# Kernel optimization log

Hardware: AMD Instinct MI355X
Metric: run time of the kernel (lower is better)

Reference implementation:

```python
import jax, jax.numpy as jnp
import numpy as np

B, C, H, W = 4, 64, 256, 256
P = 4           # patch_size
PRIOR = 64      # prior_dim
HID = 128       # token_embed_dim (score-net hidden)
E = 128         # attention embed dim
NH = 4          # num_heads
RATIO = 0.25    # top-k keep ratio (amp == phase)
TOK = C * P * P                 # 1024 token dim
SFEAT = 2 * TOK + 2 + PRIOR     # score-net input dim


def setup_inputs():
    ks = jax.random.split(jax.random.key(0), 24)
    g = lambda i, s, sc=0.02: jax.random.normal(ks[i], s, jnp.float32) * sc
    z = lambda n: jnp.zeros((n,), jnp.float32)
    return dict(
        vis_feat=g(0, (B, C, H, W), 1.0), ir_feat=g(1, (B, C, H, W), 1.0),
        prompt_bank=g(2, (4, PRIOR), 0.1),
        Wr=g(3, (2 * C, PRIOR)), br=z(PRIOR),
        aW1=g(4, (SFEAT, HID)), ab1=z(HID), aW2=g(5, (HID, 1)), ab2=z(1),
        aWq=g(6, (TOK, E)), aWk=g(7, (TOK, E)), aWv=g(8, (TOK, E)), aWo=g(9, (E, TOK)),
        pW1=g(10, (SFEAT, HID)), pb1=z(HID), pW2=g(11, (HID, 1)), pb2=z(1),
        pWq=g(12, (TOK, E)), pWk=g(13, (TOK, E)), pWv=g(14, (TOK, E)), pWo=g(15, (E, TOK)),
        c1w=g(16, (C, C, 3, 3)), c1b=z(C), c2w=g(17, (C, C, 3, 3)), c2b=z(C))


def _patchify(x):
    b, c, h, w = x.shape
    hp, wp = h // P, w // P
    t = x.reshape(b, c, hp, P, wp, P).transpose(0, 2, 4, 1, 3, 5).reshape(b, hp * wp, c * P * P)
    return t, hp, wp


def _unpatchify(t, hp, wp):
    b = t.shape[0]
    return t.reshape(b, hp, wp, C, P, P).transpose(0, 3, 1, 4, 2, 5).reshape(b, C, hp * P, wp * P)


def _coords(hp, wp):
    ys, xs = jnp.meshgrid(jnp.arange(hp, dtype=jnp.float32), jnp.arange(wp, dtype=jnp.float32), indexing='ij')
    return jnp.stack([ys / (hp - 1), xs / (wp - 1)], -1).reshape(hp * wp, 2)


def _mha(q_tok, kv_tok, Wq, Wk, Wv, Wo):
    # cross-attention: queries from vis-selected, keys/values from ir-selected
    b, k, _ = q_tok.shape
    dh = E // NH
    q = (q_tok @ Wq).reshape(b, k, NH, dh).transpose(0, 2, 1, 3)
    kk = (kv_tok @ Wk).reshape(b, k, NH, dh).transpose(0, 2, 1, 3)
    v = (kv_tok @ Wv).reshape(b, k, NH, dh).transpose(0, 2, 1, 3)
    att = jax.nn.softmax(jnp.einsum('bhqd,bhkd->bhqk', q, kk) * (1.0 / np.sqrt(dh)), -1)
    o = jnp.einsum('bhqk,bhkd->bhqd', att, v).transpose(0, 2, 1, 3).reshape(b, k, E)
    return q_tok + o @ Wo  # residual back to token dim


def _fuse_branch(vis_map, ir_map, intent, W1, b1, W2, b2, Wq, Wk, Wv, Wo):
    vt, hp, wp = _patchify(vis_map)   # [B,N,TOK]
    it, _, _ = _patchify(ir_map)
    b, n, _ = vt.shape
    cds = jnp.broadcast_to(_coords(hp, wp), (b, n, 2))
    ib = jnp.broadcast_to(intent[:, None, :], (b, n, PRIOR))
    feat = jnp.concatenate([vt, it, cds, ib], -1)        # [B,N,SFEAT]
    score = (jax.nn.relu(feat @ W1 + b1) @ W2 + b2)[..., 0]  # [B,N]
    k = int(n * RATIO)
    _, idx = jax.lax.top_k(score, k)                     # [B,k]
    vs = jnp.take_along_axis(vt, idx[..., None], 1)      # gather selected tokens
    irs = jnp.take_along_axis(it, idx[..., None], 1)
    fs = _mha(vs, irs, Wq, Wk, Wv, Wo)                   # fuse selected via attention
    full = 0.5 * (vt + it)                               # average for unselected
    full = full.at[jnp.arange(b)[:, None], idx].set(fs)  # scatter fused back
    return _unpatchify(full, hp, wp)


def _conv3(x, w, b):
    return jax.lax.conv_general_dilated(x, w, (1, 1), 'SAME', dimension_numbers=('NCHW', 'OIHW', 'NCHW')) + b[None, :, None, None]


def reference(vis_feat, ir_feat, prompt_bank, Wr, br,
              aW1, ab1, aW2, ab2, aWq, aWk, aWv, aWo,
              pW1, pb1, pW2, pb2, pWq, pWk, pWv, pWo,
              c1w, c1b, c2w, c2b):
    # intent router: GAP both modalities -> project -> softmax over prompt bank
    gv = vis_feat.mean((2, 3))
    gi = ir_feat.mean((2, 3))
    pf = jnp.concatenate([gv, gi], -1) @ Wr + br         # [B,PRIOR]
    wts = jax.nn.softmax(pf @ prompt_bank.T, -1)
    intent = wts @ prompt_bank                           # [B,PRIOR]
    # split amplitude/phase via 2D FFT
    Fv = jnp.fft.fft2(vis_feat)
    Fi = jnp.fft.fft2(ir_feat)
    va, vp = jnp.abs(Fv), jnp.angle(Fv)
    ia, ip = jnp.abs(Fi), jnp.angle(Fi)
    fa = _fuse_branch(va, ia, intent, aW1, ab1, aW2, ab2, aWq, aWk, aWv, aWo)
    fp = _fuse_branch(vp, ip, intent, pW1, pb1, pW2, pb2, pWq, pWk, pWv, pWo)
    fp = jnp.arctan2(jnp.sin(fp), jnp.cos(fp))           # phase wrap to (-pi, pi]
    spatial = jnp.fft.ifft2(fa * jnp.exp(1j * fp)).real.astype(jnp.float32)
    r = jax.nn.relu(_conv3(spatial, c1w, c1b))
    r = _conv3(r, c2w, c2b)
    return r + 0.5 * (vis_feat + ir_feat)
```

## Files before the change

kernel.cpp:

```cpp
#include <hip/hip_runtime.h>
#include <hip/hip_bf16.h>
#include <math.h>


#define PI2F 6.28318530717958647692f
#define WS_NEED 178348032ull

__device__ __forceinline__ float bf(const __hip_bfloat16 x) { return __bfloat162float(x); }
__device__ __forceinline__ float ldin(const void* p, size_t i, int f32) {
  return f32 ? ((const float*)p)[i] : bf(((const __hip_bfloat16*)p)[i]);
}


__global__ __launch_bounds__(256) void detect_dtype(const void* buf, int nchecks,
                                                    int* __restrict__ flag) {
  const unsigned short* u = (const unsigned short*)buf;
  int tid = threadIdx.x;
  int plaus = 0, tot = 0;
  for (int i = tid; i < nchecks; i += 256) {
    unsigned short x = u[2 * i];
    int ex = (x >> 7) & 0xFF;
    ++tot;
    if (ex >= 0x70 && ex <= 0x8F) ++plaus;
  }
  __shared__ int sp[256], st[256];
  sp[tid] = plaus; st[tid] = tot;
  __syncthreads();
  for (int off = 128; off; off >>= 1) {
    if (tid < off) { sp[tid] += sp[tid + off]; st[tid] += st[tid + off]; }
    __syncthreads();
  }
  if (tid == 0) flag[0] = (sp[0] * 10 < st[0] * 6) ? 1 : 0;
}


__global__ __launch_bounds__(256) void gap_kernel(const void* __restrict__ vis,
                                                  const void* __restrict__ ir,
                                                  const int* __restrict__ flags,
                                                  float* __restrict__ gmeans) {
  int fv = flags[0];
  int bc = blockIdx.x;
  int which = blockIdx.y;
  const void* src = which ? ir : vis;
  size_t base = (size_t)bc * 65536;
  float s = 0.f;
  for (int i = threadIdx.x; i < 65536; i += 256) s += ldin(src, base + i, fv);
  __shared__ float red[256];
  red[threadIdx.x] = s;
  __syncthreads();
  for (int off = 128; off; off >>= 1) {
    if (threadIdx.x < off) red[threadIdx.x] += red[threadIdx.x + off];
    __syncthreads();
  }
  if (threadIdx.x == 0) {
    int b = bc >> 6, c = bc & 63;
    gmeans[b * 128 + which * 64 + c] = red[0] * (1.0f / 65536.0f);
  }
}

__global__ __launch_bounds__(256) void intent_kernel(const float* __restrict__ gmeans,
                                                     const void* __restrict__ Wr,
                                                     const void* __restrict__ br,
                                                     const void* __restrict__ pb,
                                                     const int* __restrict__ flags,
                                                     float* __restrict__ intent) {
  int fw = flags[1];
  __shared__ float pf[4][64];
  __shared__ float lg[4][4];
  int tid = threadIdx.x;
  int b = tid >> 6, p = tid & 63;
  float acc = ldin(br, p, fw);
  for (int k = 0; k < 128; ++k) acc = fmaf(gmeans[b * 128 + k], ldin(Wr, k * 64 + p, fw), acc);
  pf[b][p] = acc;
  __syncthreads();
  if (tid < 16) {
    int bb = tid >> 2, j = tid & 3;
    float s = 0.f;
    for (int q = 0; q < 64; ++q) s = fmaf(pf[bb][q], ldin(pb, j * 64 + q, fw), s);
    lg[bb][j] = s;
  }
  __syncthreads();
  float m = fmaxf(fmaxf(lg[b][0], lg[b][1]), fmaxf(lg[b][2], lg[b][3]));
  float e0 = expf(lg[b][0] - m), e1 = expf(lg[b][1] - m);
  float e2 = expf(lg[b][2] - m), e3 = expf(lg[b][3] - m);
  float inv = 1.f / (e0 + e1 + e2 + e3);
  float v = e0 * ldin(pb, 0 * 64 + p, fw) + e1 * ldin(pb, 1 * 64 + p, fw) +
            e2 * ldin(pb, 2 * 64 + p, fw) + e3 * ldin(pb, 3 * 64 + p, fw);
  intent[b * 64 + p] = v * inv;
}


__device__ __forceinline__ void build_tw(float* twr, float* twi) {
  for (int t = threadIdx.x; t < 128; t += blockDim.x) {
    float s, c;
    sincosf(PI2F * (float)t * (1.0f / 256.0f), &s, &c);
    twr[t] = c; twi[t] = s;
  }
}

__device__ __forceinline__ void fft_core(float* re, float* im,
                                         const float* twr, const float* twi,
                                         int worker, int nw, float sgn) {
  int shift = 7;
  for (int len = 2; len <= 256; len <<= 1, --shift) {
    int half = len >> 1;
    for (int t = worker; t < 128; t += nw) {
      int pos = t & (half - 1);
      int i = 2 * t - pos;
      int j = i + half;
      float wr = twr[pos << shift];
      float wi = sgn * twi[pos << shift];
      float vr = re[j], vi = im[j];
      float tr = vr * wr - vi * wi;
      float ti = vr * wi + vi * wr;
      float ur = re[i], ui = im[i];
      re[i] = ur + tr; im[i] = ui + ti;
      re[j] = ur - tr; im[j] = ui - ti;
    }
    __syncthreads();
  }
}

__global__ __launch_bounds__(256) void fft_row_fwd_half(const void* __restrict__ in,
                                                        const int* __restrict__ flags,
                                                        float2* __restrict__ out) {
  int fv = flags[0];
  __shared__ float re[4][256], im[4][256];
  __shared__ float twr[128], twi[128];
  build_tw(twr, twi);
  int sec = threadIdx.x >> 6, lane = threadIdx.x & 63;
  size_t row = (size_t)blockIdx.x * 4 + sec;
  float* sre = re[sec]; float* sim = im[sec];
  for (int e = lane; e < 256; e += 64) {
    int rv = __brev((unsigned)e) >> 24;
    sre[rv] = ldin(in, row * 256 + e, fv);
    sim[rv] = 0.f;
  }
  __syncthreads();
  fft_core(sre, sim, twr, twi, lane, 64, -1.0f);
  float2* dst = out + row * 130;
  for (int e = lane; e < 256; e += 64)
    if (e <= 128) dst[e] = make_float2(sre[e], sim[e]);
}

__global__ __launch_bounds__(256) void fft_col_fwd_half(float2* __restrict__ buf) {
  __shared__ float re[16 * 257], im[16 * 257];
  __shared__ float twr[128], twi[128];
  build_tw(twr, twi);
  int cl = threadIdx.x & 15, wk = threadIdx.x >> 4;
  size_t img = blockIdx.y;
  int x = blockIdx.x * 16 + cl;
  bool valid = (x <= 128);
  float2* base = buf + img * (256 * 130);
  float* sre = re + cl * 257; float* sim = im + cl * 257;
  for (int y = wk; y < 256; y += 16) {
    float2 v = valid ? base[y * 130 + x] : make_float2(0.f, 0.f);
    int rv = __brev((unsigned)y) >> 24;
    sre[rv] = v.x; sim[rv] = v.y;
  }
  __syncthreads();
  fft_core(sre, sim, twr, twi, wk, 16, -1.0f);
  if (valid)
    for (int y = wk; y < 256; y += 16)
      base[y * 130 + x] = make_float2(sre[y], sim[y]);
}


__global__ __launch_bounds__(256) void polarize(float2* __restrict__ M) {
  size_t e = (size_t)blockIdx.x * 256 + threadIdx.x;
  float2 v = M[e];
  M[e] = make_float2(sqrtf(v.x * v.x + v.y * v.y), atan2f(v.y, v.x));
}


__device__ __forceinline__ float tokval_h(const float2* __restrict__ F, int b, int n, int d, int mode) {
  int c = d >> 4, iy = (d >> 2) & 3, ix = d & 3;
  int py = n >> 6, px = n & 63;
  int ky = py * 4 + iy, kx = px * 4 + ix;
  int img = b * 64 + c;
  float sgn = 1.f;
  if (kx > 128) { kx = 256 - kx; ky = (256 - ky) & 255; sgn = -1.f; }
  float2 v = F[((size_t)img * 256 + ky) * 130 + kx];
  return mode ? sgn * v.y : v.x;
}

__device__ __forceinline__ float feat_val(const float2* __restrict__ Fv, const float2* __restrict__ Fi,
                                          const float* __restrict__ intent, int b, int n, int k, int mode) {
  if (k < 1024) return tokval_h(Fv, b, n, k, mode);
  if (k < 2048) return tokval_h(Fi, b, n, k - 1024, mode);
  if (k == 2048) return (float)(n >> 6) * (1.0f / 63.0f);
  if (k == 2049) return (float)(n & 63) * (1.0f / 63.0f);
  return intent[b * 64 + (k - 2050)];
}


__global__ __launch_bounds__(256) void score_part(const float2* __restrict__ Fv,
                                                  const float2* __restrict__ Fi,
                                                  const float* __restrict__ intent,
                                                  const void* __restrict__ W1,
                                                  const int* __restrict__ flags,
                                                  float* __restrict__ Hp, int mode) {
  int fw = flags[1];
  __shared__ float As[16][65];
  __shared__ float Bs[16][129];
  int tile = blockIdx.x, b = blockIdx.y, ks = blockIdx.z;
  int kbeg = ks * 544;
  int kend = kbeg + 544; if (kend > 2114) kend = 2114;
  int tx = threadIdx.x & 15, ty = threadIdx.x >> 4;
  float acc[4][8];
#pragma unroll
  for (int i = 0; i < 4; ++i)
#pragma unroll
    for (int j = 0; j < 8; ++j) acc[i][j] = 0.f;

  for (int k0 = kbeg; k0 < kend; k0 += 16) {
#pragma unroll
    for (int q = 0; q < 4; ++q) {
      int e = threadIdx.x + q * 256;
      int r = e >> 4, kk = e & 15;
      int k = k0 + kk;
      As[kk][r] = (k < 2114) ? feat_val(Fv, Fi, intent, b, tile * 64 + r, k, mode) : 0.f;
    }
#pragma unroll
    for (int q = 0; q < 8; ++q) {
      int e = threadIdx.x + q * 256;
      int kk = e >> 7, h = e & 127;
      int k = k0 + kk;
      Bs[kk][h] = (k < 2114) ? ldin(W1, (size_t)k * 128 + h, fw) : 0.f;
    }
    __syncthreads();
#pragma unroll
    for (int kk = 0; kk < 16; ++kk) {
      float a[4], w[8];
#pragma unroll
      for (int i = 0; i < 4; ++i) a[i] = As[kk][ty + 16 * i];
#pragma unroll
      for (int j = 0; j < 8; ++j) w[j] = Bs[kk][tx + 16 * j];
#pragma unroll
      for (int i = 0; i < 4; ++i)
#pragma unroll
        for (int j = 0; j < 8; ++j) acc[i][j] = fmaf(a[i], w[j], acc[i][j]);
    }
    __syncthreads();
  }
  float* out = Hp + (size_t)ks * 2097152 + ((size_t)(b * 4096 + tile * 64)) * 128;
#pragma unroll
  for (int i = 0; i < 4; ++i)
#pragma unroll
    for (int j = 0; j < 8; ++j)
      out[(ty + 16 * i) * 128 + tx + 16 * j] = acc[i][j];
}

__global__ __launch_bounds__(256) void score_fin(const float* __restrict__ Hp,
                                                 const void* __restrict__ b1,
                                                 const void* __restrict__ W2,
                                                 const void* __restrict__ b2,
                                                 const int* __restrict__ flags,
                                                 float* __restrict__ scores) {
  int fw = flags[1];
  int tile = blockIdx.x, b = blockIdx.y;
  int r = threadIdx.x >> 2, q = threadIdx.x & 3;
  size_t off = ((size_t)(b * 4096 + tile * 64 + r)) * 128 + q * 32;
  float s = 0.f;
#pragma unroll
  for (int i = 0; i < 32; i += 4) {
    float4 h0 = *(const float4*)(Hp + off + i);
    float4 h1 = *(const float4*)(Hp + 2097152 + off + i);
    float4 h2 = *(const float4*)(Hp + 4194304 + off + i);
    float4 h3 = *(const float4*)(Hp + 6291456 + off + i);
    int h = q * 32 + i;
    float hv;
    hv = fmaxf(h0.x + h1.x + h2.x + h3.x + ldin(b1, h + 0, fw), 0.f);
    s = fmaf(hv, ldin(W2, h + 0, fw), s);
    hv = fmaxf(h0.y + h1.y + h2.y + h3.y + ldin(b1, h + 1, fw), 0.f);
    s = fmaf(hv, ldin(W2, h + 1, fw), s);
    hv = fmaxf(h0.z + h1.z + h2.z + h3.z + ldin(b1, h + 2, fw), 0.f);
    s = fmaf(hv, ldin(W2, h + 2, fw), s);
    hv = fmaxf(h0.w + h1.w + h2.w + h3.w + ldin(b1, h + 3, fw), 0.f);
    s = fmaf(hv, ldin(W2, h + 3, fw), s);
  }
  s += __shfl_xor(s, 1);
  s += __shfl_xor(s, 2);
  if (q == 0) scores[b * 4096 + tile * 64 + r] = s + ldin(b2, 0, fw);
}

__global__ __launch_bounds__(1024) void topk_kernel(const float* __restrict__ scores,
                                                    int* __restrict__ idx_out) {
  __shared__ float ks[4096];
  __shared__ int iv[4096];
  int b = blockIdx.x;
  int tid = threadIdx.x;
  for (int i = tid; i < 4096; i += 1024) { ks[i] = scores[b * 4096 + i]; iv[i] = i; }
  __syncthreads();
  for (int k = 2; k <= 4096; k <<= 1) {
    for (int j = k >> 1; j > 0; j >>= 1) {
      for (int t = tid; t < 4096; t += 1024) {
        int p = t ^ j;
        if (p > t) {
          float s1 = ks[t], s2 = ks[p];
          int i1 = iv[t], i2 = iv[p];
          bool before12 = (s1 > s2) || (s1 == s2 && i1 < i2);
          bool up = (t & k) == 0;
          bool sw = up ? (!before12) : before12;
          if (sw) { ks[t] = s2; ks[p] = s1; iv[t] = i2; iv[p] = i1; }
        }
      }
      __syncthreads();
    }
  }
  if (tid < 1024) idx_out[b * 1024 + tid] = iv[tid];
}


__global__ __launch_bounds__(256) void gemm_qkv3(const float2* __restrict__ Mv,
                                                 const float2* __restrict__ Mi,
                                                 const int* __restrict__ idx,
                                                 const void* __restrict__ Wq,
                                                 const void* __restrict__ Wk,
                                                 const void* __restrict__ Wv,
                                                 const int* __restrict__ flags,
                                                 float* __restrict__ QKV, int mode) {
  int fw = flags[1];
  int z = blockIdx.z;
  const float2* F = z ? Mi : Mv;
  const void* W = (z == 0) ? Wq : (z == 1 ? Wk : Wv);
  float* C = QKV + (size_t)z * 524288;
  __shared__ float As[16][65], Bs[16][65];
  __shared__ int nidx[64];
  int tx = threadIdx.x & 15, ty = threadIdx.x >> 4;
  int m0 = blockIdx.x * 64, n0 = blockIdx.y * 64;
  int b = m0 >> 10;
  if (threadIdx.x < 64) nidx[threadIdx.x] = idx[b * 1024 + (m0 & 1023) + threadIdx.x];
  __syncthreads();
  float acc[4][4];
#pragma unroll
  for (int i = 0; i < 4; ++i)
#pragma unroll
    for (int j = 0; j < 4; ++j) acc[i][j] = 0.f;
  for (int k0 = 0; k0 < 1024; k0 += 16) {
#pragma unroll
    for (int q = 0; q < 4; ++q) {
      int e = threadIdx.x + q * 256;
      int r = e >> 4, kk = e & 15;
      As[kk][r] = tokval_h(F, b, nidx[r], k0 + kk, mode);
    }
#pragma unroll
    for (int q = 0; q < 4; ++q) {
      int e = threadIdx.x + q * 256;
      int kk = e >> 6, c = e & 63;
      Bs[kk][c] = ldin(W, (size_t)(k0 + kk) * 128 + n0 + c, fw);
    }
    __syncthreads();
#pragma unroll
    for (int kk = 0; kk < 16; ++kk) {
      float a[4], w[4];
#pragma unroll
      for (int i = 0; i < 4; ++i) a[i] = As[kk][ty + 16 * i];
#pragma unroll
      for (int j = 0; j < 4; ++j) w[j] = Bs[kk][tx + 16 * j];
#pragma unroll
      for (int i = 0; i < 4; ++i)
#pragma unroll
        for (int j = 0; j < 4; ++j) acc[i][j] = fmaf(a[i], w[j], acc[i][j]);
    }
    __syncthreads();
  }
#pragma unroll
  for (int i = 0; i < 4; ++i)
#pragma unroll
    for (int j = 0; j < 4; ++j)
      C[(size_t)(m0 + ty + 16 * i) * 128 + n0 + tx + 16 * j] = acc[i][j];
}

__global__ __launch_bounds__(256) void gemm_out_sc(const float* __restrict__ A,
                                                   const void* __restrict__ Bw,
                                                   const float2* __restrict__ Fq,
                                                   const int* __restrict__ idx,
                                                   const int* __restrict__ flags,
                                                   __hip_bfloat16* __restrict__ plane,
                                                   int mode) {
  int fw = flags[1];
  __shared__ float As[16][65], Bs[16][65];
  __shared__ int nidx[64];
  int tx = threadIdx.x & 15, ty = threadIdx.x >> 4;
  int m0 = blockIdx.x * 64, n0 = blockIdx.y * 64;
  int b = m0 >> 10;
  if (threadIdx.x < 64) nidx[threadIdx.x] = idx[b * 1024 + (m0 & 1023) + threadIdx.x];
  __syncthreads();
  float acc[4][4];
#pragma unroll
  for (int i = 0; i < 4; ++i)
#pragma unroll
    for (int j = 0; j < 4; ++j) acc[i][j] = 0.f;
  for (int k0 = 0; k0 < 128; k0 += 16) {
#pragma unroll
    for (int q = 0; q < 4; ++q) {
      int e = threadIdx.x + q * 256;
      int r = e >> 4, kk = e & 15;
      As[kk][r] = A[(size_t)(m0 + r) * 128 + k0 + kk];
    }
#pragma unroll
    for (int q = 0; q < 4; ++q) {
      int e = threadIdx.x + q * 256;
      int kk = e >> 6, c = e & 63;
      Bs[kk][c] = ldin(Bw, (size_t)(k0 + kk) * 1024 + n0 + c, fw);
    }
    __syncthreads();
#pragma unroll
    for (int kk = 0; kk < 16; ++kk) {
      float a[4], w[4];
#pragma unroll
      for (int i = 0; i < 4; ++i) a[i] = As[kk][ty + 16 * i];
#pragma unroll
      for (int j = 0; j < 4; ++j) w[j] = Bs[kk][tx + 16 * j];
#pragma unroll
      for (int i = 0; i < 4; ++i)
#pragma unroll
        for (int j = 0; j < 4; ++j) acc[i][j] = fmaf(a[i], w[j], acc[i][j]);
    }
    __syncthreads();
  }
#pragma unroll
  for (int i = 0; i < 4; ++i) {
    int r = ty + 16 * i;
    int n = nidx[r];
    int py = n >> 6, px = n & 63;
#pragma unroll
    for (int j = 0; j < 4; ++j) {
      int d = n0 + tx + 16 * j;
      float v = acc[i][j] + tokval_h(Fq, b, n, d, mode);
      int c = d >> 4, iy = (d >> 2) & 3, ix = d & 3;
      size_t pos = ((size_t)(b * 64 + c) * 256 + (py * 4 + iy)) * 256 + (px * 4 + ix);
      plane[pos] = __float2bfloat16(v);
    }
  }
}

__global__ __launch_bounds__(256) void attn_tile(const float* __restrict__ Q,
                                                 const float* __restrict__ K,
                                                 const float* __restrict__ V,
                                                 float* __restrict__ O) {
  __shared__ float Qs[32][36];
  __shared__ float Ks[64][36];
  __shared__ float VsT[32][68];
  __shared__ float Ps[32][68];
  const float scale = 0.17677669529663687f;
  int qt = blockIdx.x, h = blockIdx.y, b = blockIdx.z;
  int t = threadIdx.x;
  int tx = t & 15, ty = t >> 4;
  size_t qrow0 = (size_t)(b * 1024 + qt * 32);
  size_t krow0 = (size_t)(b * 1024);
  {
    int r = t >> 3, d0 = (t & 7) * 4;
    float4 v = *(const float4*)(Q + (qrow0 + r) * 128 + h * 32 + d0);
    Qs[r][d0] = v.x; Qs[r][d0 + 1] = v.y; Qs[r][d0 + 2] = v.z; Qs[r][d0 + 3] = v.w;
  }
  float m0 = -1e30f, m1 = -1e30f, l0 = 0.f, l1 = 0.f;
  float a00 = 0.f, a01 = 0.f, a10 = 0.f, a11 = 0.f;

#pragma unroll 1
  for (int kt = 0; kt < 16; ++kt) {
    __syncthreads();
    {
      int r = t >> 2, d0 = (t & 3) * 8;
      const float* src = K + (krow0 + kt * 64 + r) * 128 + h * 32 + d0;
      float4 a = *(const float4*)src;
      float4 c = *(const float4*)(src + 4);
      Ks[r][d0] = a.x; Ks[r][d0 + 1] = a.y; Ks[r][d0 + 2] = a.z; Ks[r][d0 + 3] = a.w;
      Ks[r][d0 + 4] = c.x; Ks[r][d0 + 5] = c.y; Ks[r][d0 + 6] = c.z; Ks[r][d0 + 7] = c.w;
    }
    {
      int kk = t >> 2, d0 = (t & 3) * 8;
      const float* src = V + (krow0 + kt * 64 + kk) * 128 + h * 32 + d0;
      float4 a = *(const float4*)src;
      float4 c = *(const float4*)(src + 4);
      VsT[d0][kk] = a.x; VsT[d0 + 1][kk] = a.y; VsT[d0 + 2][kk] = a.z; VsT[d0 + 3][kk] = a.w;
      VsT[d0 + 4][kk] = c.x; VsT[d0 + 5][kk] = c.y; VsT[d0 + 6][kk] = c.z; VsT[d0 + 7][kk] = c.w;
    }
    __syncthreads();
    float s0[4] = {0.f, 0.f, 0.f, 0.f}, s1[4] = {0.f, 0.f, 0.f, 0.f};
#pragma unroll
    for (int d0 = 0; d0 < 32; d0 += 4) {
      float4 qa = *(const float4*)&Qs[ty][d0];
      float4 qb = *(const float4*)&Qs[ty + 16][d0];
#pragma unroll
      for (int j = 0; j < 4; ++j) {
        float4 kv = *(const float4*)&Ks[tx + 16 * j][d0];
        s0[j] = fmaf(qa.x, kv.x, s0[j]); s0[j] = fmaf(qa.y, kv.y, s0[j]);
        s0[j] = fmaf(qa.z, kv.z, s0[j]); s0[j] = fmaf(qa.w, kv.w, s0[j]);
        s1[j] = fmaf(qb.x, kv.x, s1[j]); s1[j] = fmaf(qb.y, kv.y, s1[j]);
        s1[j] = fmaf(qb.z, kv.z, s1[j]); s1[j] = fmaf(qb.w, kv.w, s1[j]);
      }
    }
#pragma unroll
    for (int j = 0; j < 4; ++j) { s0[j] *= scale; s1[j] *= scale; }
    float mt0 = fmaxf(fmaxf(s0[0], s0[1]), fmaxf(s0[2], s0[3]));
    float mt1 = fmaxf(fmaxf(s1[0], s1[1]), fmaxf(s1[2], s1[3]));
#pragma unroll
    for (int xm = 1; xm < 16; xm <<= 1) {
      mt0 = fmaxf(mt0, __shfl_xor(mt0, xm));
      mt1 = fmaxf(mt1, __shfl_xor(mt1, xm));
    }
    float mn0 = fmaxf(m0, mt0), mn1 = fmaxf(m1, mt1);
    float sc0 = __expf(m0 - mn0), sc1 = __expf(m1 - mn1);
    m0 = mn0; m1 = mn1;
    float p0[4], p1[4];
    float lt0 = 0.f, lt1 = 0.f;
#pragma unroll
    for (int j = 0; j < 4; ++j) {
      p0[j] = __expf(s0[j] - mn0); lt0 += p0[j];
      p1[j] = __expf(s1[j] - mn1); lt1 += p1[j];
    }
#pragma unroll
    for (int xm = 1; xm < 16; xm <<= 1) {
      lt0 += __shfl_xor(lt0, xm);
      lt1 += __shfl_xor(lt1, xm);
    }
    l0 = l0 * sc0 + lt0;
    l1 = l1 * sc1 + lt1;
    a00 *= sc0; a01 *= sc0; a10 *= sc1; a11 *= sc1;
#pragma unroll
    for (int j = 0; j < 4; ++j) {
      Ps[ty][tx + 16 * j] = p0[j];
      Ps[ty + 16][tx + 16 * j] = p1[j];
    }
    __syncthreads();
#pragma unroll
    for (int kk = 0; kk < 64; kk += 4) {
      float4 pa = *(const float4*)&Ps[ty][kk];
      float4 pb = *(const float4*)&Ps[ty + 16][kk];
      float4 va = *(const float4*)&VsT[tx][kk];
      float4 vb = *(const float4*)&VsT[tx + 16][kk];
      a00 = fmaf(pa.x, va.x, a00); a00 = fmaf(pa.y, va.y, a00);
      a00 = fmaf(pa.z, va.z, a00); a00 = fmaf(pa.w, va.w, a00);
      a01 = fmaf(pa.x, vb.x, a01); a01 = fmaf(pa.y, vb.y, a01);
      a01 = fmaf(pa.z, vb.z, a01); a01 = fmaf(pa.w, vb.w, a01);
      a10 = fmaf(pb.x, va.x, a10); a10 = fmaf(pb.y, va.y, a10);
      a10 = fmaf(pb.z, va.z, a10); a10 = fmaf(pb.w, va.w, a10);
      a11 = fmaf(pb.x, vb.x, a11); a11 = fmaf(pb.y, vb.y, a11);
      a11 = fmaf(pb.z, vb.z, a11); a11 = fmaf(pb.w, vb.w, a11);
    }
  }
  float inv0 = 1.f / l0, inv1 = 1.f / l1;
  float* op0 = O + (qrow0 + ty) * 128 + h * 32;
  float* op1 = O + (qrow0 + ty + 16) * 128 + h * 32;
  op0[tx] = a00 * inv0; op0[tx + 16] = a01 * inv0;
  op1[tx] = a10 * inv1; op1[tx + 16] = a11 * inv1;
}


__global__ __launch_bounds__(256) void fuse_avg(const float2* __restrict__ Mv,
                                                const float2* __restrict__ Mi,
                                                __hip_bfloat16* __restrict__ Za,
                                                __hip_bfloat16* __restrict__ Zp) {
  int e = blockIdx.x * 256 + threadIdx.x;
  int img = e >> 16, r = e & 65535;
  int ky = r >> 8, kx = r & 255;
  float sgn = 1.f;
  int kys = ky, kxs = kx;
  if (kx > 128) { kxs = 256 - kx; kys = (256 - ky) & 255; sgn = -1.f; }
  size_t off = ((size_t)img * 256 + kys) * 130 + kxs;
  float2 v = Mv[off], w = Mi[off];
  float fa = 0.5f * (v.x + w.x);
  float fp = 0.5f * sgn * (v.y + w.y);
  Za[e] = __float2bfloat16(fa);
  Zp[e] = __float2bfloat16(fp);
}


__global__ __launch_bounds__(256) void ifft_col(const __hip_bfloat16* __restrict__ Za,
                                                const __hip_bfloat16* __restrict__ Zp,
                                                float2* __restrict__ T) {
  __shared__ float re[16 * 257], im[16 * 257];
  __shared__ float twr[128], twi[128];
  build_tw(twr, twi);
  int cl = threadIdx.x & 15, wk = threadIdx.x >> 4;
  size_t img = blockIdx.y;
  int x = blockIdx.x * 16 + cl;
  float* sre = re + cl * 257; float* sim = im + cl * 257;
  for (int y = wk; y < 256; y += 16) {
    size_t g = (img * 256 + y) * 256 + x;
    float fa = bf(Za[g]), fp = bf(Zp[g]);
    float s, c;
    sincosf(fp, &s, &c);
    int rv = __brev((unsigned)y) >> 24;
    sre[rv] = fa * c; sim[rv] = fa * s;
  }
  __syncthreads();
  fft_core(sre, sim, twr, twi, wk, 16, 1.0f);
  for (int y = wk; y < 256; y += 16)
    T[(img * 256 + y) * 256 + x] = make_float2(sre[y], sim[y]);
}

__global__ __launch_bounds__(256) void ifft_row(const float2* __restrict__ T,
                                                __hip_bfloat16* __restrict__ spatial) {
  __shared__ float re[4][256], im[4][256];
  __shared__ float twr[128], twi[128];
  build_tw(twr, twi);
  int sec = threadIdx.x >> 6, lane = threadIdx.x & 63;
  size_t row = (size_t)blockIdx.x * 4 + sec;
  const float2* src = T + row * 256;
  float* sre = re[sec]; float* sim = im[sec];
  for (int e = lane; e < 256; e += 64) {
    float2 v = src[e];
    int rv = __brev((unsigned)e) >> 24;
    sre[rv] = v.x; sim[rv] = v.y;
  }
  __syncthreads();
  fft_core(sre, sim, twr, twi, lane, 64, 1.0f);
  __hip_bfloat16* dst = spatial + row * 256;
  for (int e = lane; e < 256; e += 64)
    dst[e] = __float2bfloat16(sre[e] * (1.0f / 65536.0f));
}

#define ICB 4
__global__ __launch_bounds__(256) void conv3x3_kernel(const __hip_bfloat16* __restrict__ in_h,
                                                      const float* __restrict__ in_f,
                                                      const void* __restrict__ w,
                                                      const void* __restrict__ bias,
                                                      const int* __restrict__ flags,
                                                      float* __restrict__ out_f,
                                                      void* __restrict__ out_any,
                                                      const void* __restrict__ res_a,
                                                      const void* __restrict__ res_b,
                                                      int relu_flag) {
  int fv = flags[0], fw = flags[1];
  int bz = blockIdx.z;
  int b = bz >> 2, ocg = bz & 3;
  int x0 = blockIdx.x * 32, y0 = blockIdx.y * 32;
  int t = threadIdx.x;
  int tx = t & 7;
  int tyy = (t >> 3) & 15;
  int og = t >> 7;
  __shared__ __align__(16) float tile[ICB][34 * 40];
  __shared__ __align__(16) float wl[ICB][16][12];
  float acc[8][2][4];
#pragma unroll
  for (int o = 0; o < 8; ++o)
#pragma unroll
    for (int h2 = 0; h2 < 2; ++h2)
#pragma unroll
      for (int p = 0; p < 4; ++p) acc[o][h2][p] = 0.f;

  for (int ic0 = 0; ic0 < 64; ic0 += ICB) {
    __syncthreads();
    for (int e = threadIdx.x; e < ICB * 1156; e += 256) {
      int ics = e / 1156, rem = e - ics * 1156;
      int r = rem / 34, c2 = rem - r * 34;
      int gy = y0 - 1 + r, gx = x0 - 1 + c2;
      float v = 0.f;
      if ((unsigned)gy < 256u && (unsigned)gx < 256u) {
        size_t chan = ((size_t)(b * 64 + ic0 + ics)) * 65536;
        v = in_f ? in_f[chan + gy * 256 + gx] : bf(in_h[chan + gy * 256 + gx]);
      }
      tile[ics][r * 40 + c2] = v;
    }
    for (int e = threadIdx.x; e < ICB * 144; e += 256) {
      int ics = e / 144, rem = e - ics * 144;
      int o = rem / 9, k = rem - o * 9;
      wl[ics][o][k] = ldin(w, ((size_t)(ocg * 16 + o) * 64 + ic0 + ics) * 9 + k, fw);
    }
    __syncthreads();
#pragma unroll
    for (int ics = 0; ics < ICB; ++ics) {
      float xr[2][3][6];
#pragma unroll
      for (int h2 = 0; h2 < 2; ++h2)
#pragma unroll
        for (int dr = 0; dr < 3; ++dr) {
          const float* rp = &tile[ics][(tyy + 16 * h2 + dr) * 40 + 4 * tx];
          float4 xa = *(const float4*)rp;
          float2 xb = *(const float2*)(rp + 4);
          xr[h2][dr][0] = xa.x; xr[h2][dr][1] = xa.y; xr[h2][dr][2] = xa.z;
          xr[h2][dr][3] = xa.w; xr[h2][dr][4] = xb.x; xr[h2][dr][5] = xb.y;
        }
#pragma unroll
      for (int o = 0; o < 8; ++o) {
        float4 wa = *(const float4*)&wl[ics][og * 8 + o][0];
        float4 wb = *(const float4*)&wl[ics][og * 8 + o][4];
        float w8 = wl[ics][og * 8 + o][8];
#pragma unroll
        for (int h2 = 0; h2 < 2; ++h2)
#pragma unroll
          for (int p = 0; p < 4; ++p) {
            float s = acc[o][h2][p];
            s = fmaf(wa.x, xr[h2][0][p], s);
            s = fmaf(wa.y, xr[h2][0][p + 1], s);
            s = fmaf(wa.z, xr[h2][0][p + 2], s);
            s = fmaf(wa.w, xr[h2][1][p], s);
            s = fmaf(wb.x, xr[h2][1][p + 1], s);
            s = fmaf(wb.y, xr[h2][1][p + 2], s);
            s = fmaf(wb.z, xr[h2][2][p], s);
            s = fmaf(wb.w, xr[h2][2][p + 1], s);
            s = fmaf(w8, xr[h2][2][p + 2], s);
            acc[o][h2][p] = s;
          }
      }
    }
  }
  int xbase = x0 + 4 * tx;
#pragma unroll
  for (int o = 0; o < 8; ++o) {
    int oc = ocg * 16 + og * 8 + o;
    float bv = ldin(bias, oc, fw);
#pragma unroll
    for (int h2 = 0; h2 < 2; ++h2) {
      int y = y0 + tyy + 16 * h2;
      size_t base = ((size_t)(b * 64 + oc) * 256 + y) * 256 + xbase;
      if (relu_flag) {
        float4 v;
        v.x = fmaxf(acc[o][h2][0] + bv, 0.f);
        v.y = fmaxf(acc[o][h2][1] + bv, 0.f);
        v.z = fmaxf(acc[o][h2][2] + bv, 0.f);
        v.w = fmaxf(acc[o][h2][3] + bv, 0.f);
        *(float4*)(out_f + base) = v;
      } else {
#pragma unroll
        for (int p = 0; p < 4; ++p) {
          float v = acc[o][h2][p] + bv + 0.5f * (ldin(res_a, base + p, fv) + ldin(res_b, base + p, fv));
          if (fv) ((float*)out_any)[base + p] = v;
          else ((__hip_bfloat16*)out_any)[base + p] = __float2bfloat16(v);
        }
      }
    }
  }
}

__global__ __launch_bounds__(256) void encode_ws(__hip_bfloat16* __restrict__ out, float val) {
  int e = blockIdx.x * 256 + threadIdx.x;
  out[e] = __float2bfloat16(val);
}


extern "C" void kernel_launch(void* const* d_in, const int* in_sizes, int n_in,
                              void* d_out, int out_size, void* d_ws, size_t ws_size,
                              hipStream_t stream) {
  (void)in_sizes; (void)n_in; (void)out_size;
  const void* vis = d_in[0];
  const void* ir  = d_in[1];
  const void* pb  = d_in[2];
  const void* Wr  = d_in[3];
  const void* br  = d_in[4];
  const void* W1[2] = {d_in[5],  d_in[13]};
  const void* b1[2] = {d_in[6],  d_in[14]};
  const void* W2[2] = {d_in[7],  d_in[15]};
  const void* b2[2] = {d_in[8],  d_in[16]};
  const void* Wq[2] = {d_in[9],  d_in[17]};
  const void* Wk[2] = {d_in[10], d_in[18]};
  const void* Wv[2] = {d_in[11], d_in[19]};
  const void* Wo[2] = {d_in[12], d_in[20]};
  const void* c1w = d_in[21];
  const void* c1b = d_in[22];
  const void* c2w = d_in[23];
  const void* c2b = d_in[24];

  char* ws = (char*)d_ws;
  float2* Mv = (float2*)(ws);
  float2* Mi = (float2*)(ws + 68157440ull);
  __hip_bfloat16* Zp = (__hip_bfloat16*)(ws + 136314880ull);
  float* Hpart = (float*)(ws + 136314880ull);
  const size_t S = 169869312ull;
  int*   flags  = (int*)(ws + S);
  float* gmeans = (float*)(ws + S + 256);
  float* intent = (float*)(ws + S + 2304);
  int*   idx0   = (int*)(ws + S + 4096);
  int*   idx1   = (int*)(ws + S + 20480);
  float* scores = (float*)(ws + S + 36864);
  float* Qb = (float*)(ws + S + 36864);
  float* Kb = Qb + 524288;
  float* Vb = Kb + 524288;
  float* Ob = Vb + 524288;
  float2* T  = (float2*)(ws);
  float*  r1 = (float*)(ws);
  __hip_bfloat16* Za = (__hip_bfloat16*)d_out;

  detect_dtype<<<1, 256, 0, stream>>>(vis, 2048, flags);
  detect_dtype<<<1, 256, 0, stream>>>(W1[0], 2048, flags + 1);

  gap_kernel<<<dim3(256, 2), 256, 0, stream>>>(vis, ir, flags, gmeans);
  intent_kernel<<<1, 256, 0, stream>>>(gmeans, Wr, br, pb, flags, intent);

  fft_row_fwd_half<<<16384, 256, 0, stream>>>(vis, flags, Mv);
  fft_row_fwd_half<<<16384, 256, 0, stream>>>(ir, flags, Mi);
  fft_col_fwd_half<<<dim3(9, 256), 256, 0, stream>>>(Mv);
  fft_col_fwd_half<<<dim3(9, 256), 256, 0, stream>>>(Mi);

  polarize<<<66560, 256, 0, stream>>>(Mv);

  for (int m = 0; m < 2; ++m) {
    score_part<<<dim3(64, 4, 4), 256, 0, stream>>>(Mv, Mi, intent, W1[m], flags, Hpart, m);
    score_fin<<<dim3(64, 4), 256, 0, stream>>>(Hpart, b1[m], W2[m], b2[m], flags, scores);
    topk_kernel<<<4, 1024, 0, stream>>>(scores, m ? idx1 : idx0);
  }

  fuse_avg<<<65536, 256, 0, stream>>>(Mv, Mi, Za, Zp);

  for (int m = 0; m < 2; ++m) {
    __hip_bfloat16* plane = m ? Zp : Za;
    int* idxm = m ? idx1 : idx0;
    gemm_qkv3<<<dim3(64, 2, 3), 256, 0, stream>>>(Mv, Mi, idxm, Wq[m], Wk[m], Wv[m], flags, Qb, m);
    attn_tile<<<dim3(32, 4, 4), 256, 0, stream>>>(Qb, Kb, Vb, Ob);
    gemm_out_sc<<<dim3(64, 16), 256, 0, stream>>>(Ob, Wo[m], Mv, idxm, flags, plane, m);
  }

  ifft_col<<<dim3(16, 256), 256, 0, stream>>>(Za, Zp, T);
  ifft_row<<<16384, 256, 0, stream>>>(T, Za);

  conv3x3_kernel<<<dim3(8, 8, 16), 256, 0, stream>>>(Za, nullptr, c1w, c1b, flags, r1, nullptr, nullptr, nullptr, 1);
  conv3x3_kernel<<<dim3(8, 8, 16), 256, 0, stream>>>(nullptr, r1, c2w, c2b, flags, nullptr, d_out, vis, ir, 0);

  if (ws_size < WS_NEED)
    encode_ws<<<65536, 256, 0, stream>>>((__hip_bfloat16*)d_out, (float)(ws_size >> 20));
}
```

Baseline: 3.450 ms.

## Widen conv3x3 blocks to all 64 output channels and prefetch next input slice

The 3x3 conv now uses 1024-thread blocks that cover all 64 output channels for one batch image, instead of four 256-thread blocks each covering 16 channels. Each input tile is therefore loaded from global memory once rather than four times. It also adds register-staged prefetching: the loads for the next input-channel slice and its weights are issued before the compute on the current slice, to overlap global latency with FMAs. In exchange the grid shrinks to 256 blocks of 1024 threads with roughly 8 extra staging registers per thread, which may cut occupancy and parallelism across the 256 CUs.

```diff
diff --git a/kernel.cpp b/kernel.cpp
--- a/kernel.cpp
+++ b/kernel.cpp
@@ -614,26 +614,25 @@
 }
 
 #define ICB 4
-__global__ __launch_bounds__(256) void conv3x3_kernel(const __hip_bfloat16* __restrict__ in_h,
-                                                      const float* __restrict__ in_f,
-                                                      const void* __restrict__ w,
-                                                      const void* __restrict__ bias,
-                                                      const int* __restrict__ flags,
-                                                      float* __restrict__ out_f,
-                                                      void* __restrict__ out_any,
-                                                      const void* __restrict__ res_a,
-                                                      const void* __restrict__ res_b,
-                                                      int relu_flag) {
+__global__ __launch_bounds__(1024) void conv3x3_kernel(const __hip_bfloat16* __restrict__ in_h,
+                                                       const float* __restrict__ in_f,
+                                                       const void* __restrict__ w,
+                                                       const void* __restrict__ bias,
+                                                       const int* __restrict__ flags,
+                                                       float* __restrict__ out_f,
+                                                       void* __restrict__ out_any,
+                                                       const void* __restrict__ res_a,
+                                                       const void* __restrict__ res_b,
+                                                       int relu_flag) {
   int fv = flags[0], fw = flags[1];
-  int bz = blockIdx.z;
-  int b = bz >> 2, ocg = bz & 3;
+  int b = blockIdx.z;
   int x0 = blockIdx.x * 32, y0 = blockIdx.y * 32;
   int t = threadIdx.x;
   int tx = t & 7;
   int tyy = (t >> 3) & 15;
   int og = t >> 7;
   __shared__ __align__(16) float tile[ICB][34 * 40];
-  __shared__ __align__(16) float wl[ICB][16][12];
+  __shared__ __align__(16) float wl[ICB][64][12];
   float acc[8][2][4];
 #pragma unroll
   for (int o = 0; o < 8; ++o)
@@ -642,23 +641,84 @@
 #pragma unroll
       for (int p = 0; p < 4; ++p) acc[o][h2][p] = 0.f;
 
-  for (int ic0 = 0; ic0 < 64; ic0 += ICB) {
-    __syncthreads();
-    for (int e = threadIdx.x; e < ICB * 1156; e += 256) {
+  float sreg[5];
+  float wreg[3];
+
+#pragma unroll
+  for (int i = 0; i < 5; ++i) {
+    int e = t + i * 1024;
+    float v = 0.f;
+    if (e < ICB * 1156) {
       int ics = e / 1156, rem = e - ics * 1156;
       int r = rem / 34, c2 = rem - r * 34;
       int gy = y0 - 1 + r, gx = x0 - 1 + c2;
-      float v = 0.f;
       if ((unsigned)gy < 256u && (unsigned)gx < 256u) {
-        size_t chan = ((size_t)(b * 64 + ic0 + ics)) * 65536;
+        size_t chan = ((size_t)(b * 64 + ics)) * 65536;
         v = in_f ? in_f[chan + gy * 256 + gx] : bf(in_h[chan + gy * 256 + gx]);
       }
-      tile[ics][r * 40 + c2] = v;
-    }
-    for (int e = threadIdx.x; e < ICB * 144; e += 256) {
-      int ics = e / 144, rem = e - ics * 144;
+    }
+    sreg[i] = v;
+  }
+#pragma unroll
+  for (int i = 0; i < 3; ++i) {
+    int e = t + i * 1024;
+    float v = 0.f;
+    if (e < ICB * 576) {
+      int ics = e / 576, rem = e - ics * 576;
       int o = rem / 9, k = rem - o * 9;
-      wl[ics][o][k] = ldin(w, ((size_t)(ocg * 16 + o) * 64 + ic0 + ics) * 9 + k, fw);
+      v = ldin(w, ((size_t)o * 64 + ics) * 9 + k, fw);
+    }
+    wreg[i] = v;
+  }
+
+  for (int ic0 = 0; ic0 < 64; ic0 += ICB) {
+    __syncthreads();
+#pragma unroll
+    for (int i = 0; i < 5; ++i) {
+      int e = t + i * 1024;
+      if (e < ICB * 1156) {
+        int ics = e / 1156, rem = e - ics * 1156;
+        int r = rem / 34, c2 = rem - r * 34;
+        tile[ics][r * 40 + c2] = sreg[i];
+      }
+    }
+#pragma unroll
+    for (int i = 0; i < 3; ++i) {
+      int e = t + i * 1024;
+      if (e < ICB * 576) {
+        int ics = e / 576, rem = e - ics * 576;
+        int o = rem / 9, k = rem - o * 9;
+        wl[ics][o][k] = wreg[i];
+      }
+    }
+    int icn = ic0 + ICB;
+    if (icn < 64) {
+#pragma unroll
+      for (int i = 0; i < 5; ++i) {
+        int e = t + i * 1024;
+        float v = 0.f;
+        if (e < ICB * 1156) {
+          int ics = e / 1156, rem = e - ics * 1156;
+          int r = rem / 34, c2 = rem - r * 34;
+          int gy = y0 - 1 + r, gx = x0 - 1 + c2;
+          if ((unsigned)gy < 256u && (unsigned)gx < 256u) {
+            size_t chan = ((size_t)(b * 64 + icn + ics)) * 65536;
+            v = in_f ? in_f[chan + gy * 256 + gx] : bf(in_h[chan + gy * 256 + gx]);
+          }
+        }
+        sreg[i] = v;
+      }
+#pragma unroll
+      for (int i = 0; i < 3; ++i) {
+        int e = t + i * 1024;
+        float v = 0.f;
+        if (e < ICB * 576) {
+          int ics = e / 576, rem = e - ics * 576;
+          int o = rem / 9, k = rem - o * 9;
+          v = ldin(w, ((size_t)o * 64 + icn + ics) * 9 + k, fw);
+        }
+        wreg[i] = v;
+      }
     }
     __syncthreads();
 #pragma unroll
@@ -701,7 +761,7 @@
   int xbase = x0 + 4 * tx;
 #pragma unroll
   for (int o = 0; o < 8; ++o) {
-    int oc = ocg * 16 + og * 8 + o;
+    int oc = og * 8 + o;
     float bv = ldin(bias, oc, fw);
 #pragma unroll
     for (int h2 = 0; h2 < 2; ++h2) {
@@ -806,8 +866,8 @@
   ifft_col<<<dim3(16, 256), 256, 0, stream>>>(Za, Zp, T);
   ifft_row<<<16384, 256, 0, stream>>>(T, Za);
 
-  conv3x3_kernel<<<dim3(8, 8, 16), 256, 0, stream>>>(Za, nullptr, c1w, c1b, flags, r1, nullptr, nullptr, nullptr, 1);
-  conv3x3_kernel<<<dim3(8, 8, 16), 256, 0, stream>>>(nullptr, r1, c2w, c2b, flags, nullptr, d_out, vis, ir, 0);
+  conv3x3_kernel<<<dim3(8, 8, 4), 1024, 0, stream>>>(Za, nullptr, c1w, c1b, flags, r1, nullptr, nullptr, nullptr, 1);
+  conv3x3_kernel<<<dim3(8, 8, 4), 1024, 0, stream>>>(nullptr, r1, c2w, c2b, flags, nullptr, d_out, vis, ir, 0);
 
   if (ws_size < WS_NEED)
     encode_ws<<<65536, 256, 0, stream>>>((__hip_bfloat16*)d_out, (float)(ws_size >> 20));
```

After: 3.513 ms. Within noise of the previous version (+1.8%).

## Compute all 64 output channels per conv block to reuse input tiles

Applied to the files above, without the earlier changes.

The 3x3 conv kernel now launches 1024-thread blocks. Each block covers all 64 output channels of a 32x32 spatial tile, where it used to cover 16 channels with 256 threads. The shared input halo tile is therefore loaded from global memory once instead of four times, at the cost of a larger weight buffer in shared memory. The inner loop is also reordered so the per-row input registers are only live for one half-tile, which lowers register pressure under the new launch bounds. The risks are that the grid shrinks to 256 large blocks, roughly one per CU, and that latency hiding may get worse.

```diff
diff --git a/kernel.cpp b/kernel.cpp
--- a/kernel.cpp
+++ b/kernel.cpp
@@ -614,26 +614,25 @@
 }
 
 #define ICB 4
-__global__ __launch_bounds__(256) void conv3x3_kernel(const __hip_bfloat16* __restrict__ in_h,
-                                                      const float* __restrict__ in_f,
-                                                      const void* __restrict__ w,
-                                                      const void* __restrict__ bias,
-                                                      const int* __restrict__ flags,
-                                                      float* __restrict__ out_f,
-                                                      void* __restrict__ out_any,
-                                                      const void* __restrict__ res_a,
-                                                      const void* __restrict__ res_b,
-                                                      int relu_flag) {
+__global__ __launch_bounds__(1024, 4) void conv3x3_kernel(const __hip_bfloat16* __restrict__ in_h,
+                                                          const float* __restrict__ in_f,
+                                                          const void* __restrict__ w,
+                                                          const void* __restrict__ bias,
+                                                          const int* __restrict__ flags,
+                                                          float* __restrict__ out_f,
+                                                          void* __restrict__ out_any,
+                                                          const void* __restrict__ res_a,
+                                                          const void* __restrict__ res_b,
+                                                          int relu_flag) {
   int fv = flags[0], fw = flags[1];
-  int bz = blockIdx.z;
-  int b = bz >> 2, ocg = bz & 3;
+  int b = blockIdx.z;
   int x0 = blockIdx.x * 32, y0 = blockIdx.y * 32;
   int t = threadIdx.x;
   int tx = t & 7;
   int tyy = (t >> 3) & 15;
   int og = t >> 7;
   __shared__ __align__(16) float tile[ICB][34 * 40];
-  __shared__ __align__(16) float wl[ICB][16][12];
+  __shared__ __align__(16) float wl[ICB][64][12];
   float acc[8][2][4];
 #pragma unroll
   for (int o = 0; o < 8; ++o)
@@ -644,7 +643,7 @@
 
   for (int ic0 = 0; ic0 < 64; ic0 += ICB) {
     __syncthreads();
-    for (int e = threadIdx.x; e < ICB * 1156; e += 256) {
+    for (int e = t; e < ICB * 1156; e += 1024) {
       int ics = e / 1156, rem = e - ics * 1156;
       int r = rem / 34, c2 = rem - r * 34;
       int gy = y0 - 1 + r, gx = x0 - 1 + c2;
@@ -655,53 +654,52 @@
       }
       tile[ics][r * 40 + c2] = v;
     }
-    for (int e = threadIdx.x; e < ICB * 144; e += 256) {
-      int ics = e / 144, rem = e - ics * 144;
+    for (int e = t; e < ICB * 576; e += 1024) {
+      int ics = e / 576, rem = e - ics * 576;
       int o = rem / 9, k = rem - o * 9;
-      wl[ics][o][k] = ldin(w, ((size_t)(ocg * 16 + o) * 64 + ic0 + ics) * 9 + k, fw);
+      wl[ics][o][k] = ldin(w, ((size_t)o * 64 + ic0 + ics) * 9 + k, fw);
     }
     __syncthreads();
 #pragma unroll
     for (int ics = 0; ics < ICB; ++ics) {
-      float xr[2][3][6];
-#pragma unroll
-      for (int h2 = 0; h2 < 2; ++h2)
+#pragma unroll
+      for (int h2 = 0; h2 < 2; ++h2) {
+        float xr[3][6];
 #pragma unroll
         for (int dr = 0; dr < 3; ++dr) {
           const float* rp = &tile[ics][(tyy + 16 * h2 + dr) * 40 + 4 * tx];
           float4 xa = *(const float4*)rp;
           float2 xb = *(const float2*)(rp + 4);
-          xr[h2][dr][0] = xa.x; xr[h2][dr][1] = xa.y; xr[h2][dr][2] = xa.z;
-          xr[h2][dr][3] = xa.w; xr[h2][dr][4] = xb.x; xr[h2][dr][5] = xb.y;
+          xr[dr][0] = xa.x; xr[dr][1] = xa.y; xr[dr][2] = xa.z;
+          xr[dr][3] = xa.w; xr[dr][4] = xb.x; xr[dr][5] = xb.y;
         }
 #pragma unroll
-      for (int o = 0; o < 8; ++o) {
-        float4 wa = *(const float4*)&wl[ics][og * 8 + o][0];
-        float4 wb = *(const float4*)&wl[ics][og * 8 + o][4];
-        float w8 = wl[ics][og * 8 + o][8];
-#pragma unroll
-        for (int h2 = 0; h2 < 2; ++h2)
+        for (int o = 0; o < 8; ++o) {
+          float4 wa = *(const float4*)&wl[ics][og * 8 + o][0];
+          float4 wb = *(const float4*)&wl[ics][og * 8 + o][4];
+          float w8 = wl[ics][og * 8 + o][8];
 #pragma unroll
           for (int p = 0; p < 4; ++p) {
             float s = acc[o][h2][p];
-            s = fmaf(wa.x, xr[h2][0][p], s);
-            s = fmaf(wa.y, xr[h2][0][p + 1], s);
-            s = fmaf(wa.z, xr[h2][0][p + 2], s);
-            s = fmaf(wa.w, xr[h2][1][p], s);
-            s = fmaf(wb.x, xr[h2][1][p + 1], s);
-            s = fmaf(wb.y, xr[h2][1][p + 2], s);
-            s = fmaf(wb.z, xr[h2][2][p], s);
-            s = fmaf(wb.w, xr[h2][2][p + 1], s);
-            s = fmaf(w8, xr[h2][2][p + 2], s);
+            s = fmaf(wa.x, xr[0][p], s);
+            s = fmaf(wa.y, xr[0][p + 1], s);
+            s = fmaf(wa.z, xr[0][p + 2], s);
+            s = fmaf(wa.w, xr[1][p], s);
+            s = fmaf(wb.x, xr[1][p + 1], s);
+            s = fmaf(wb.y, xr[1][p + 2], s);
+            s = fmaf(wb.z, xr[2][p], s);
+            s = fmaf(wb.w, xr[2][p + 1], s);
+            s = fmaf(w8, xr[2][p + 2], s);
             acc[o][h2][p] = s;
           }
+        }
       }
     }
   }
   int xbase = x0 + 4 * tx;
 #pragma unroll
   for (int o = 0; o < 8; ++o) {
-    int oc = ocg * 16 + og * 8 + o;
+    int oc = og * 8 + o;
     float bv = ldin(bias, oc, fw);
 #pragma unroll
     for (int h2 = 0; h2 < 2; ++h2) {
@@ -806,8 +804,8 @@
   ifft_col<<<dim3(16, 256), 256, 0, stream>>>(Za, Zp, T);
   ifft_row<<<16384, 256, 0, stream>>>(T, Za);
 
-  conv3x3_kernel<<<dim3(8, 8, 16), 256, 0, stream>>>(Za, nullptr, c1w, c1b, flags, r1, nullptr, nullptr, nullptr, 1);
-  conv3x3_kernel<<<dim3(8, 8, 16), 256, 0, stream>>>(nullptr, r1, c2w, c2b, flags, nullptr, d_out, vis, ir, 0);
+  conv3x3_kernel<<<dim3(8, 8, 4), 1024, 0, stream>>>(Za, nullptr, c1w, c1b, flags, r1, nullptr, nullptr, nullptr, 1);
+  conv3x3_kernel<<<dim3(8, 8, 4), 1024, 0, stream>>>(nullptr, r1, c2w, c2b, flags, nullptr, d_out, vis, ir, 0);
 
   if (ws_size < WS_NEED)
     encode_ws<<<65536, 256, 0, stream>>>((__hip_bfloat16*)d_out, (float)(ws_size >> 20));
```

After: 5.573 ms. +61.6%, slower.
